# Kernel optimization log

Measured on AMD Instinct MI355X. Metric: run time of the kernel, lower is better.

Reference implementation:

```python
import jax, jax.numpy as jnp
import numpy as np

N_NODES = 100000
N_EDGES = 640000
IN_DIM = 128
OUT_DIM = 128
EDGE_DIM = 4
N_GROUPS = 8
EPS = 1e-5


def setup_inputs() -> dict:
    key = jax.random.key(0)
    ks = jax.random.split(key, 9)
    x = jax.random.normal(ks[0], (N_NODES, IN_DIM), dtype=jnp.float32)
    edge_index = jax.random.randint(ks[1], (2, N_EDGES), 0, N_NODES, dtype=jnp.int64)
    edge_attr = jax.random.normal(ks[2], (N_EDGES, EDGE_DIM), dtype=jnp.float32)
    d_in = 2 * IN_DIM + EDGE_DIM
    # Linear layers (kaiming-uniform-ish init scale)
    W1 = jax.random.uniform(ks[3], (d_in, OUT_DIM), jnp.float32, -1, 1) / np.sqrt(d_in)
    b1 = jax.random.uniform(ks[4], (OUT_DIM,), jnp.float32, -1, 1) / np.sqrt(d_in)
    W2 = jax.random.uniform(ks[5], (OUT_DIM, OUT_DIM), jnp.float32, -1, 1) / np.sqrt(OUT_DIM)
    b2 = jax.random.uniform(ks[6], (OUT_DIM,), jnp.float32, -1, 1) / np.sqrt(OUT_DIM)
    gn_gamma = jnp.ones((OUT_DIM,), jnp.float32)
    gn_beta = jnp.zeros((OUT_DIM,), jnp.float32)
    return {"x": x, "edge_index": edge_index, "edge_attr": edge_attr,
            "W1": W1, "b1": b1, "gn_gamma": gn_gamma, "gn_beta": gn_beta,
            "W2": W2, "b2": b2}


def group_norm(h, gamma, beta):
    # h: [E, C]; normalize each row per group of C//N_GROUPS channels
    E, C = h.shape
    hg = h.reshape(E, N_GROUPS, C // N_GROUPS)
    mean = jnp.mean(hg, axis=-1, keepdims=True)
    var = jnp.mean(jnp.square(hg - mean), axis=-1, keepdims=True)
    hg = (hg - mean) * jax.lax.rsqrt(var + EPS)
    return hg.reshape(E, C) * gamma + beta


def reference(x, edge_index, edge_attr, W1, b1, gn_gamma, gn_beta, W2, b2):
    src, dst = edge_index[0], edge_index[1]
    # gather endpoint features: [E, 2*in_dim + edge_dim]
    feat = jnp.concatenate([x[dst], x[src], edge_attr], axis=-1)
    h = feat @ W1 + b1                      # [E, out_dim]
    h = group_norm(h, gn_gamma, gn_beta)
    h = jax.nn.silu(h)
    messages = h @ W2 + b2                  # [E, out_dim]
    out = jax.ops.segment_sum(messages, dst, num_segments=x.shape[0])
    count = jax.ops.segment_sum(jnp.ones((messages.shape[0], 1), x.dtype), dst,
                                num_segments=x.shape[0])
    return out / jnp.maximum(count, 1.0)
```

## Files before the change

### kernel.cpp

```cpp
#include <hip/hip_runtime.h>
#include <hip/hip_bf16.h>

#define NNODES 100000
#define NEDGES 640000
#define DIM 128
#define GS 16
#define EB 64
#define NSCAN_BLOCKS ((NNODES + 255) / 256)
#define G1_BLOCKS ((NNODES + 63) / 64)

typedef __attribute__((ext_vector_type(8))) short short8;
typedef __attribute__((ext_vector_type(4))) float f32x4;

__device__ __forceinline__ ushort f2bf(float f) {
    __hip_bfloat16 h = __float2bfloat16(f);
    return *reinterpret_cast<ushort*>(&h);
}
__device__ __forceinline__ float bf2f(ushort u) {
    union { unsigned int i; float f; } v; v.i = ((unsigned int)u) << 16; return v.f;
}

__global__ void zero_kernel(float* __restrict__ out, int* __restrict__ hist) {
    long step = (long)gridDim.x * blockDim.x;
    long i0 = (long)blockIdx.x * blockDim.x + threadIdx.x;
    const long total = (long)NNODES * DIM;
    for (long i = i0; i < total; i += step) out[i] = 0.f;
    for (long i = i0; i < NNODES; i += step) hist[i] = 0;
}

__global__ __launch_bounds__(256) void node_gemm1(const float* __restrict__ x,
                                                  const float* __restrict__ W1,
                                                  ushort* __restrict__ xab) {
    __shared__ __align__(16) char xt[64 * 256];
    const int tid  = threadIdx.x;
    const int lane = tid & 63;
    const int w    = tid >> 6;
    const int lr   = lane & 15;
    const int lg   = lane >> 4;
    const int m0   = blockIdx.x * 64;
    const int mtMax = (m0 + 64 <= NNODES) ? 4 : 2;

    const int koff = (w >= 2) ? 128 : 0;
    short8 bfrag[4][4];
    #pragma unroll
    for (int nt = 0; nt < 4; ++nt) {
        const int cc = (w & 1) * 64 + nt * 16 + lr;
        #pragma unroll
        for (int kt = 0; kt < 4; ++kt) {
            const int kb = koff + kt * 32 + lg * 8;
            short8 f;
            #pragma unroll
            for (int j = 0; j < 8; ++j) f[j] = (short)f2bf(W1[(long)(kb + j) * DIM + cc]);
            bfrag[nt][kt] = f;
        }
    }

    {
        const int r  = tid >> 2;
        const int kq = (tid & 3) * 32;
        if (m0 + r < NNODES) {
            const float* xr = &x[(long)(m0 + r) * DIM + kq];
            ushort tmp[32];
            #pragma unroll
            for (int j = 0; j < 32; ++j) tmp[j] = f2bf(xr[j]);
            #pragma unroll
            for (int i = 0; i < 4; ++i) {
                int byte = r * 256 + kq * 2 + i * 16;
                byte ^= (r & 7) << 4;
                *(short8*)(xt + byte) = *(short8*)&tmp[i * 8];
            }
        }
    }
    __syncthreads();

    const int colBase = w * 64;
    for (int mt = 0; mt < mtMax; ++mt) {
        short8 afrag[4];
        #pragma unroll
        for (int kt = 0; kt < 4; ++kt) {
            const int row = mt * 16 + lr;
            int byte = row * 256 + (kt * 4 + lg) * 16;
            byte ^= (row & 7) << 4;
            afrag[kt] = *(short8*)(xt + byte);
        }
        f32x4 acc[4] = {};
        #pragma unroll
        for (int nt = 0; nt < 4; ++nt)
            #pragma unroll
            for (int kt = 0; kt < 4; ++kt)
                acc[nt] = __builtin_amdgcn_mfma_f32_16x16x32_bf16(afrag[kt], bfrag[nt][kt], acc[nt], 0, 0, 0);
        #pragma unroll
        for (int nt = 0; nt < 4; ++nt) {
            const int col = colBase + nt * 16 + lr;
            #pragma unroll
            for (int r = 0; r < 4; ++r) {
                const int row = m0 + mt * 16 + lg * 4 + r;
                xab[(long)row * 256 + col] = f2bf(acc[nt][r]);
            }
        }
    }
}

__global__ void hist_kernel(const int* __restrict__ ei, int* __restrict__ hist) {
    int e = blockIdx.x * 256 + threadIdx.x;
    if (e < NEDGES) atomicAdd(&hist[ei[NEDGES + e]], 1);
}

__global__ void scan1_kernel(const int* __restrict__ hist, int* __restrict__ excl,
                             int* __restrict__ bsums) {
    __shared__ int s[256];
    int tid = threadIdx.x;
    int i = blockIdx.x * 256 + tid;
    int v = (i < NNODES) ? hist[i] : 0;
    s[tid] = v;
    __syncthreads();
    for (int o = 1; o < 256; o <<= 1) {
        int t = (tid >= o) ? s[tid - o] : 0;
        __syncthreads();
        s[tid] += t;
        __syncthreads();
    }
    if (i < NNODES) excl[i] = s[tid] - v;
    if (tid == 255) bsums[blockIdx.x] = s[255];
}

__global__ void scan2_kernel(int* __restrict__ bsums) {
    __shared__ int s[512];
    int tid = threadIdx.x;
    int v = (tid < NSCAN_BLOCKS) ? bsums[tid] : 0;
    s[tid] = v;
    __syncthreads();
    for (int o = 1; o < 512; o <<= 1) {
        int t = (tid >= o) ? s[tid - o] : 0;
        __syncthreads();
        s[tid] += t;
        __syncthreads();
    }
    if (tid < NSCAN_BLOCKS) bsums[tid] = s[tid] - v;
}

__global__ void scan3_kernel(const int* __restrict__ excl, const int* __restrict__ bsums,
                             int* __restrict__ cursor) {
    int i = blockIdx.x * 256 + threadIdx.x;
    if (i < NNODES) cursor[i] = excl[i] + bsums[blockIdx.x];
}

__global__ void scatter_kernel(const int* __restrict__ ei, int* __restrict__ cursor,
                               int* __restrict__ sorted) {
    int e = blockIdx.x * 256 + threadIdx.x;
    if (e < NEDGES) {
        int d = ei[NEDGES + e];
        int pos = atomicAdd(&cursor[d], 1);
        sorted[pos] = e;
    }
}

__global__ __launch_bounds__(256) void edge_silu_kernel(
    const ushort* __restrict__ xab,
    const int* __restrict__ ei, const float* __restrict__ ea,
    const int* __restrict__ sorted,
    const float* __restrict__ W1, const float* __restrict__ b1,
    const float* __restrict__ gamma, const float* __restrict__ beta,
    float* __restrict__ out)
{
    __shared__ __align__(16) ushort ssilu[EB * 128];
    __shared__ float w1cs[4][4][33];
    __shared__ float sb1s[4][33], sgs[4][33], sbts[4][33];
    __shared__ int   sdst[EB], ssrc[EB], seid[EB];
    __shared__ float sea[EB][4];

    const int tid = threadIdx.x;
    const int e0 = blockIdx.x * EB;

    if (tid < EB) {
        int id = sorted[e0 + tid];
        seid[tid] = id;
        sdst[tid] = ei[NEDGES + id];
        ssrc[tid] = ei[id];
        *(float4*)&sea[tid][0] = *(const float4*)&ea[(long)id * 4];
    }
    if (tid < 128) {
        int q = tid >> 5, i = tid & 31;
        sb1s[q][i] = b1[tid]; sgs[q][i] = gamma[tid]; sbts[q][i] = beta[tid];
        w1cs[0][q][i] = W1[256 * DIM + tid];
        w1cs[1][q][i] = W1[257 * DIM + tid];
        w1cs[2][q][i] = W1[258 * DIM + tid];
        w1cs[3][q][i] = W1[259 * DIM + tid];
    }
    __syncthreads();

    {
        const int e = tid >> 2;
        const int q = tid & 3;
        const int c0 = q * 32;
        const ushort* xaRow = &xab[(long)sdst[e] * 256 + c0];
        const ushort* xbRow = &xab[(long)ssrc[e] * 256 + 128 + c0];
        const float a0 = sea[e][0], a1 = sea[e][1], a2 = sea[e][2], a3 = sea[e][3];

        float v[32];
        #pragma unroll
        for (int i = 0; i < 4; ++i) {
            short8 va = *(const short8*)&xaRow[i * 8];
            short8 vb = *(const short8*)&xbRow[i * 8];
            #pragma unroll
            for (int j = 0; j < 8; ++j) {
                int idx = i * 8 + j;
                v[idx] = bf2f((ushort)va[j]) + bf2f((ushort)vb[j]) + sb1s[q][idx]
                       + a0 * w1cs[0][q][idx] + a1 * w1cs[1][q][idx]
                       + a2 * w1cs[2][q][idx] + a3 * w1cs[3][q][idx];
            }
        }

        #pragma unroll
        for (int g = 0; g < 2; ++g) {
            float sum = 0.f;
            #pragma unroll
            for (int i = 0; i < GS; ++i) sum += v[g * GS + i];
            float mean = sum * (1.f / GS);
            float var = 0.f;
            #pragma unroll
            for (int i = 0; i < GS; ++i) { float d = v[g * GS + i] - mean; var += d * d; }
            var *= (1.f / GS);
            float inv = rsqrtf(var + 1e-5f);
            #pragma unroll
            for (int i = 0; i < GS; ++i) {
                int idx = g * GS + i;
                float t = (v[idx] - mean) * inv * sgs[q][idx] + sbts[q][idx];
                v[idx] = t / (1.f + __expf(-t));
            }
        }
        ushort tmp[32];
        #pragma unroll
        for (int j = 0; j < 32; ++j) tmp[j] = f2bf(v[j]);
        #pragma unroll
        for (int i = 0; i < 4; ++i) {
            int byte = e * 256 + (c0 + i * 8) * 2;
            byte ^= (e & 7) << 4;
            *(short8*)((char*)ssilu + byte) = *(short8*)&tmp[i * 8];
        }
    }
    __syncthreads();

    {
        const int c = tid & 127;
        const int h = tid >> 7;
        const int eS = h * 32, eE = eS + 32;
        float r = 0.f;
        int cur = sdst[eS];
        for (int ee = eS; ee < eE; ++ee) {
            int d = sdst[ee];
            if (d != cur) {
                unsafeAtomicAdd(&out[(long)cur * DIM + c], r);
                r = 0.f; cur = d;
            }
            int byte = (ee * 256 + c * 2) ^ ((ee & 7) << 4);
            r += bf2f(*(const ushort*)((const char*)ssilu + byte));
        }
        unsafeAtomicAdd(&out[(long)cur * DIM + c], r);
    }
}

__global__ __launch_bounds__(256) void node_gemm2(float* __restrict__ out,
                                                  const float* __restrict__ W2,
                                                  const float* __restrict__ b2,
                                                  const int* __restrict__ hist) {
    __shared__ __align__(16) char at[64 * 256];
    __shared__ float sb2[128];
    __shared__ int scnt[64];
    const int tid  = threadIdx.x;
    const int lane = tid & 63;
    const int w    = tid >> 6;
    const int lr   = lane & 15;
    const int lg   = lane >> 4;
    const int m0   = blockIdx.x * 64;
    const int mtMax = (m0 + 64 <= NNODES) ? 4 : 2;

    short8 bfrag[2][4];
    #pragma unroll
    for (int nt = 0; nt < 2; ++nt) {
        const int cc = w * 32 + nt * 16 + lr;
        #pragma unroll
        for (int kt = 0; kt < 4; ++kt) {
            const int kb = kt * 32 + lg * 8;
            short8 f;
            #pragma unroll
            for (int j = 0; j < 8; ++j) f[j] = (short)f2bf(W2[(long)(kb + j) * DIM + cc]);
            bfrag[nt][kt] = f;
        }
    }

    if (tid < 128) sb2[tid] = b2[tid];
    if (tid < 64 && m0 + tid < NNODES) scnt[tid] = hist[m0 + tid];

    {
        const int r  = tid >> 2;
        const int kq = (tid & 3) * 32;
        if (m0 + r < NNODES) {
            const float* ar = &out[(long)(m0 + r) * DIM + kq];
            ushort tmp[32];
            #pragma unroll
            for (int j = 0; j < 32; ++j) tmp[j] = f2bf(ar[j]);
            #pragma unroll
            for (int i = 0; i < 4; ++i) {
                int byte = r * 256 + kq * 2 + i * 16;
                byte ^= (r & 7) << 4;
                *(short8*)(at + byte) = *(short8*)&tmp[i * 8];
            }
        }
    }
    __syncthreads();

    for (int mt = 0; mt < mtMax; ++mt) {
        short8 afrag[4];
        #pragma unroll
        for (int kt = 0; kt < 4; ++kt) {
            const int row = mt * 16 + lr;
            int byte = row * 256 + (kt * 4 + lg) * 16;
            byte ^= (row & 7) << 4;
            afrag[kt] = *(short8*)(at + byte);
        }
        f32x4 acc[2] = {};
        #pragma unroll
        for (int nt = 0; nt < 2; ++nt)
            #pragma unroll
            for (int kt = 0; kt < 4; ++kt)
                acc[nt] = __builtin_amdgcn_mfma_f32_16x16x32_bf16(afrag[kt], bfrag[nt][kt], acc[nt], 0, 0, 0);
        #pragma unroll
        for (int nt = 0; nt < 2; ++nt) {
            const int col = w * 32 + nt * 16 + lr;
            #pragma unroll
            for (int r = 0; r < 4; ++r) {
                const int rr = mt * 16 + lg * 4 + r;
                float cnt = (float)scnt[rr];
                float sc = 1.f / fmaxf(cnt, 1.f);
                out[(long)(m0 + rr) * DIM + col] = (acc[nt][r] + cnt * sb2[col]) * sc;
            }
        }
    }
}

extern "C" void kernel_launch(void* const* d_in, const int* in_sizes, int n_in,
                              void* d_out, int out_size, void* d_ws, size_t ws_size,
                              hipStream_t stream) {
    const float* x     = (const float*)d_in[0];
    const int*   ei    = (const int*)  d_in[1];
    const float* ea    = (const float*)d_in[2];
    const float* W1    = (const float*)d_in[3];
    const float* b1    = (const float*)d_in[4];
    const float* gamma = (const float*)d_in[5];
    const float* beta  = (const float*)d_in[6];
    const float* W2    = (const float*)d_in[7];
    const float* b2    = (const float*)d_in[8];
    float* out = (float*)d_out;

    char* ws = (char*)d_ws;
    size_t off = 0;
    ushort* xab   = (ushort*)(ws + off); off += (size_t)NNODES * 256 * sizeof(ushort);
    int*    hist  = (int*)   (ws + off); off += (size_t)NNODES * sizeof(int);
    int*    excl  = (int*)   (ws + off); off += (size_t)NNODES * sizeof(int);
    int*    cursor= (int*)   (ws + off); off += (size_t)NNODES * sizeof(int);
    int*    bsums = (int*)   (ws + off); off += 512 * sizeof(int);
    int*    sorted= (int*)   (ws + off); off += (size_t)NEDGES * sizeof(int);

    zero_kernel<<<2048, 256, 0, stream>>>(out, hist);
    node_gemm1<<<G1_BLOCKS, 256, 0, stream>>>(x, W1, xab);
    hist_kernel<<<(NEDGES + 255) / 256, 256, 0, stream>>>(ei, hist);
    scan1_kernel<<<NSCAN_BLOCKS, 256, 0, stream>>>(hist, excl, bsums);
    scan2_kernel<<<1, 512, 0, stream>>>(bsums);
    scan3_kernel<<<NSCAN_BLOCKS, 256, 0, stream>>>(excl, bsums, cursor);
    scatter_kernel<<<(NEDGES + 255) / 256, 256, 0, stream>>>(ei, cursor, sorted);
    edge_silu_kernel<<<NEDGES / EB, 256, 0, stream>>>(xab, ei, ea, sorted,
                                                      W1, b1, gamma, beta, out);
    node_gemm2<<<G1_BLOCKS, 256, 0, stream>>>(out, W2, b2, hist);
}
```

Before: 224.4 us.

## Process two edges per thread with 128-edge blocks and packed W1 edge weights

Doubles the edges per block to 128 so each thread gathers and normalizes two edges, reusing the shared-memory weight, bias and gamma/beta loads across both. The edge-attribute weights are packed into padded float4 entries. Group-norm variance now comes from a single pass over the sum and sum of squares. Segment reduction runs over 64 edges per half-block, which means fewer atomics at run boundaries. In exchange it uses more registers and LDS per block, which may lower occupancy, and the one-pass variance is slightly less numerically robust.

After: 386.5 us. +72.2%, slower.

```diff
diff --git a/kernel.cpp b/kernel.cpp
--- a/kernel.cpp
+++ b/kernel.cpp
@@ -5,7 +5,7 @@
 #define NEDGES 640000
 #define DIM 128
 #define GS 16
-#define EB 64
+#define EB 128
 #define NSCAN_BLOCKS ((NNODES + 255) / 256)
 #define G1_BLOCKS ((NNODES + 63) / 64)
 
@@ -164,79 +164,92 @@
     float* __restrict__ out)
 {
     __shared__ __align__(16) ushort ssilu[EB * 128];
-    __shared__ float w1cs[4][4][33];
-    __shared__ float sb1s[4][33], sgs[4][33], sbts[4][33];
-    __shared__ int   sdst[EB], ssrc[EB], seid[EB];
-    __shared__ float sea[EB][4];
+    __shared__ __align__(16) float4 w1ct[132];
+    __shared__ float sbb1[132], sgam[132], sbet[132];
+    __shared__ int   sdst[EB], ssrc[EB];
+    __shared__ float4 sea4[EB];
 
     const int tid = threadIdx.x;
     const int e0 = blockIdx.x * EB;
 
-    if (tid < EB) {
+    if (tid < 128) {
         int id = sorted[e0 + tid];
-        seid[tid] = id;
         sdst[tid] = ei[NEDGES + id];
         ssrc[tid] = ei[id];
-        *(float4*)&sea[tid][0] = *(const float4*)&ea[(long)id * 4];
-    }
-    if (tid < 128) {
-        int q = tid >> 5, i = tid & 31;
-        sb1s[q][i] = b1[tid]; sgs[q][i] = gamma[tid]; sbts[q][i] = beta[tid];
-        w1cs[0][q][i] = W1[256 * DIM + tid];
-        w1cs[1][q][i] = W1[257 * DIM + tid];
-        w1cs[2][q][i] = W1[258 * DIM + tid];
-        w1cs[3][q][i] = W1[259 * DIM + tid];
+        sea4[tid] = *(const float4*)&ea[(long)id * 4];
+        int c = tid;
+        int p = c + (c >> 5);
+        w1ct[p] = make_float4(W1[256 * DIM + c], W1[257 * DIM + c],
+                              W1[258 * DIM + c], W1[259 * DIM + c]);
+        sbb1[p] = b1[c]; sgam[p] = gamma[c]; sbet[p] = beta[c];
     }
     __syncthreads();
 
     {
-        const int e = tid >> 2;
+        const int eA = tid >> 2;
+        const int eBt = eA + 64;
         const int q = tid & 3;
         const int c0 = q * 32;
-        const ushort* xaRow = &xab[(long)sdst[e] * 256 + c0];
-        const ushort* xbRow = &xab[(long)ssrc[e] * 256 + 128 + c0];
-        const float a0 = sea[e][0], a1 = sea[e][1], a2 = sea[e][2], a3 = sea[e][3];
-
-        float v[32];
+        const int pBase = c0 + q;
+        const ushort* xaA = &xab[(long)sdst[eA] * 256 + c0];
+        const ushort* xbA = &xab[(long)ssrc[eA] * 256 + 128 + c0];
+        const ushort* xaB = &xab[(long)sdst[eBt] * 256 + c0];
+        const ushort* xbB = &xab[(long)ssrc[eBt] * 256 + 128 + c0];
+        const float4 aA = sea4[eA], aB = sea4[eBt];
+
+        float vA[32], vB[32];
         #pragma unroll
         for (int i = 0; i < 4; ++i) {
-            short8 va = *(const short8*)&xaRow[i * 8];
-            short8 vb = *(const short8*)&xbRow[i * 8];
+            short8 gaA = *(const short8*)&xaA[i * 8];
+            short8 gbA = *(const short8*)&xbA[i * 8];
+            short8 gaB = *(const short8*)&xaB[i * 8];
+            short8 gbB = *(const short8*)&xbB[i * 8];
             #pragma unroll
             for (int j = 0; j < 8; ++j) {
-                int idx = i * 8 + j;
-                v[idx] = bf2f((ushort)va[j]) + bf2f((ushort)vb[j]) + sb1s[q][idx]
-                       + a0 * w1cs[0][q][idx] + a1 * w1cs[1][q][idx]
-                       + a2 * w1cs[2][q][idx] + a3 * w1cs[3][q][idx];
+                const int idx = i * 8 + j;
+                const float4 w = w1ct[pBase + idx];
+                const float bb = sbb1[pBase + idx];
+                float base = bb;
+                float tA = base + aA.x * w.x + aA.y * w.y + aA.z * w.z + aA.w * w.w;
+                float tB = base + aB.x * w.x + aB.y * w.y + aB.z * w.z + aB.w * w.w;
+                vA[idx] = tA + bf2f((ushort)gaA[j]) + bf2f((ushort)gbA[j]);
+                vB[idx] = tB + bf2f((ushort)gaB[j]) + bf2f((ushort)gbB[j]);
             }
         }
 
         #pragma unroll
         for (int g = 0; g < 2; ++g) {
-            float sum = 0.f;
-            #pragma unroll
-            for (int i = 0; i < GS; ++i) sum += v[g * GS + i];
-            float mean = sum * (1.f / GS);
-            float var = 0.f;
-            #pragma unroll
-            for (int i = 0; i < GS; ++i) { float d = v[g * GS + i] - mean; var += d * d; }
-            var *= (1.f / GS);
-            float inv = rsqrtf(var + 1e-5f);
+            float sA = 0.f, qA = 0.f, sB = 0.f, qB = 0.f;
             #pragma unroll
             for (int i = 0; i < GS; ++i) {
-                int idx = g * GS + i;
-                float t = (v[idx] - mean) * inv * sgs[q][idx] + sbts[q][idx];
-                v[idx] = t / (1.f + __expf(-t));
-            }
-        }
-        ushort tmp[32];
-        #pragma unroll
-        for (int j = 0; j < 32; ++j) tmp[j] = f2bf(v[j]);
+                float a = vA[g * GS + i], b = vB[g * GS + i];
+                sA += a; qA += a * a;
+                sB += b; qB += b * b;
+            }
+            const float mA = sA * (1.f / GS), mB = sB * (1.f / GS);
+            const float varA = qA * (1.f / GS) - mA * mA;
+            const float varB = qB * (1.f / GS) - mB * mB;
+            const float iA = rsqrtf(varA + 1e-5f), iB = rsqrtf(varB + 1e-5f);
+            #pragma unroll
+            for (int i = 0; i < GS; ++i) {
+                const int idx = g * GS + i;
+                const float gm = sgam[pBase + idx], bt = sbet[pBase + idx];
+                float tA = (vA[idx] - mA) * iA * gm + bt;
+                float tB = (vB[idx] - mB) * iB * gm + bt;
+                vA[idx] = tA / (1.f + __expf(-tA));
+                vB[idx] = tB / (1.f + __expf(-tB));
+            }
+        }
+
+        ushort tA[32], tB[32];
+        #pragma unroll
+        for (int j = 0; j < 32; ++j) { tA[j] = f2bf(vA[j]); tB[j] = f2bf(vB[j]); }
         #pragma unroll
         for (int i = 0; i < 4; ++i) {
-            int byte = e * 256 + (c0 + i * 8) * 2;
-            byte ^= (e & 7) << 4;
-            *(short8*)((char*)ssilu + byte) = *(short8*)&tmp[i * 8];
+            int byteA = (eA * 256 + (c0 + i * 8) * 2) ^ ((eA & 7) << 4);
+            int byteB = (eBt * 256 + (c0 + i * 8) * 2) ^ ((eBt & 7) << 4);
+            *(short8*)((char*)ssilu + byteA) = *(short8*)&tA[i * 8];
+            *(short8*)((char*)ssilu + byteB) = *(short8*)&tB[i * 8];
         }
     }
     __syncthreads();
@@ -244,7 +257,7 @@
     {
         const int c = tid & 127;
         const int h = tid >> 7;
-        const int eS = h * 32, eE = eS + 32;
+        const int eS = h * 64, eE = eS + 64;
         float r = 0.f;
         int cur = sdst[eS];
         for (int ee = eS; ee < eE; ++ee) {
```
